# Optimization experiments

Hardware: AMD Instinct MI355X
Metric: run time of the kernel (lower is better)

Reference implementation:

```python
import jax, jax.numpy as jnp
import numpy as np

N, E, DIN, DH, DOUT, NB = 50000, 400000, 32, 128, 16, 2

def setup_inputs() -> dict:
    key = jax.random.key(0)
    ks = jax.random.split(key, 16)
    s = 0.05
    inp = {
        "inputs": jax.random.normal(ks[0], (N, DIN), jnp.float32),
        "frames": jax.random.normal(ks[1], (N, 3, 3), jnp.float32),
        "edge_index": jax.random.randint(ks[2], (2, E), 0, N, jnp.int32),
        # GraphNet in/out projections
        "win": jax.random.normal(ks[3], (DIN, DH), jnp.float32) * s,
        "bin_": jnp.zeros((DH,), jnp.float32),
        "wout": jax.random.normal(ks[4], (DH, DOUT), jnp.float32) * s,
        "bout": jnp.zeros((DOUT,), jnp.float32),
        # per-block EdgeConv params, stacked over NB blocks
        # mlp1: Linear(2*DH, DH) -> ReLU -> Linear(DH, DH) -> ReLU -> Linear(DH, DH)
        "w1a": jax.random.normal(ks[5], (NB, 2 * DH, DH), jnp.float32) * s,
        "b1a": jnp.zeros((NB, DH), jnp.float32),
        "w1b": jax.random.normal(ks[6], (NB, DH, DH), jnp.float32) * s,
        "b1b": jnp.zeros((NB, DH), jnp.float32),
        "w1c": jax.random.normal(ks[7], (NB, DH, DH), jnp.float32) * s,
        "b1c": jnp.zeros((NB, DH), jnp.float32),
        # mlp2: Linear(DH, DH) -> ReLU -> Linear(DH, DH)
        "w2a": jax.random.normal(ks[8], (NB, DH, DH), jnp.float32) * s,
        "b2a": jnp.zeros((NB, DH), jnp.float32),
        "w2b": jax.random.normal(ks[9], (NB, DH, DH), jnp.float32) * s,
        "b2b": jnp.zeros((NB, DH), jnp.float32),
    }
    return inp


def reference(inputs, frames, edge_index, win, bin_, wout, bout,
              w1a, b1a, w1b, b1b, w1c, b1c, w2a, b2a, w2b, b2b):
    src = edge_index[0]  # j: message source
    dst = edge_index[1]  # i: aggregation target (PyG convention)
    x = inputs @ win + bin_  # [N, DH]
    for b in range(NB):
        x_j = x[src]  # [E, DH] gather
        x_i = x[dst]  # [E, DH] gather
        m = jnp.concatenate([x_j, x_i], axis=-1)  # [E, 2*DH]
        m = jax.nn.relu(m @ w1a[b] + b1a[b])
        m = jax.nn.relu(m @ w1b[b] + b1b[b])
        m = m @ w1c[b] + b1c[b]  # [E, DH]
        agg = jax.ops.segment_sum(m, dst, num_segments=N)  # aggr='add'
        h = jax.nn.relu(agg @ w2a[b] + b2a[b])
        x = h @ w2b[b] + b2b[b]
    return x @ wout + bout  # [N, DOUT]
```

## Files before the change

kernel.cpp:

```cpp
#include <hip/hip_runtime.h>

#define NN 50000
#define NE 400000
#define DIN 32
#define DH  128
#define DOUT 16
#define NB  2
#define NBLK 49
#define NTILE (NE / 64)

typedef _Float16 half8 __attribute__((ext_vector_type(8)));
typedef _Float16 half4 __attribute__((ext_vector_type(4)));
typedef float    f32x4 __attribute__((ext_vector_type(4)));

#define FENCE() asm volatile("s_waitcnt lgkmcnt(0)" ::: "memory")
#define MFMA16(a, b, c) __builtin_amdgcn_mfma_f32_16x16x32_f16((a), (b), (c), 0, 0, 0)

__global__ void k_node_proj(const float* __restrict__ inp,
                            const float* __restrict__ win,
                            const float* __restrict__ bin,
                            _Float16* __restrict__ x16) {
    int gid = blockIdx.x * blockDim.x + threadIdx.x;
    if (gid >= NN * DH) return;
    int n = gid >> 7, h = gid & 127;
    float acc = bin[h];
    const float* row = inp + (size_t)n * DIN;
#pragma unroll
    for (int k = 0; k < DIN; ++k) acc = fmaf(row[k], win[k * DH + h], acc);
    x16[gid] = (_Float16)acc;
}

__global__ void k_wprep(const float* __restrict__ w1a, const float* __restrict__ w1b,
                        const float* __restrict__ w1c, const float* __restrict__ w2a,
                        const float* __restrict__ w2b, _Float16* __restrict__ wf) {
    int c = blockIdx.x * blockDim.x + threadIdx.x;
    if (c >= NB * 12288) return;
    int b = c / 12288, r = c % 12288;
    int tt = r >> 9, rem = r & 511;
    const float* W; int t;
    if (tt < 8)       { W = w1a + (size_t)b * 2 * DH * DH; t = tt; }
    else if (tt < 12) { W = w1b + (size_t)b * DH * DH; t = tt - 8; }
    else if (tt < 16) { W = w1c + (size_t)b * DH * DH; t = tt - 12; }
    else if (tt < 20) { W = w2a + (size_t)b * DH * DH; t = tt - 16; }
    else              { W = w2b + (size_t)b * DH * DH; t = tt - 20; }
    bool perm = (tt >= 12 && tt < 16);
    int n = rem >> 6, l = rem & 63;
    int col = n * 16 + (l & 15);
    half8 v;
#pragma unroll
    for (int j = 0; j < 8; ++j) {
        int row = perm ? ((2 * t + (j >> 2)) * 16 + (l >> 4) * 4 + (j & 3))
                       : (t * 32 + (l >> 4) * 8 + j);
        v[j] = (_Float16)W[(size_t)row * DH + col];
    }
    *(half8*)(wf + (size_t)c * 8) = v;
}

__global__ void k_woutprep(const float* __restrict__ wout, _Float16* __restrict__ wf) {
    int c = threadIdx.x;
    int t = c >> 6, l = c & 63;
    half8 v;
#pragma unroll
    for (int j = 0; j < 8; ++j)
        v[j] = (_Float16)wout[(size_t)(t * 32 + (l >> 4) * 8 + j) * DOUT + (l & 15)];
    *(half8*)(wf + (size_t)c * 8) = v;
}

__global__ void k_hist(const int* __restrict__ dstI, int* __restrict__ deg) {
    int e = blockIdx.x * blockDim.x + threadIdx.x;
    if (e < NE) atomicAdd(&deg[dstI[e]], 1);
}

__global__ void __launch_bounds__(1024) k_scanA(const int* __restrict__ deg,
                                                int* __restrict__ bsum) {
    __shared__ int ws[16];
    int tid = threadIdx.x, wv = tid >> 6, l = tid & 63;
    int i = blockIdx.x * 1024 + tid;
    int v = (i < NN) ? deg[i] : 0;
#pragma unroll
    for (int off = 32; off; off >>= 1) v += __shfl_down(v, off);
    if (l == 0) ws[wv] = v;
    __syncthreads();
    if (tid == 0) {
        int s = 0;
#pragma unroll
        for (int k = 0; k < 16; ++k) s += ws[k];
        bsum[blockIdx.x] = s;
    }
}

__global__ void k_scanB(const int* __restrict__ bsum, int* __restrict__ boff) {
    int l = threadIdx.x;
    int v = (l < NBLK) ? bsum[l] : 0;
    int s = v;
#pragma unroll
    for (int off = 1; off < 64; off <<= 1) {
        int t = __shfl_up(s, off);
        if (l >= off) s += t;
    }
    if (l < NBLK) boff[l] = s - v;
}

__global__ void __launch_bounds__(1024) k_scanC(const int* __restrict__ deg,
                                                const int* __restrict__ boff,
                                                int* __restrict__ cur) {
    __shared__ int ws[16];
    int tid = threadIdx.x, wv = tid >> 6, l = tid & 63;
    int i = blockIdx.x * 1024 + tid;
    int v = (i < NN) ? deg[i] : 0;
    int s = v;
#pragma unroll
    for (int off = 1; off < 64; off <<= 1) {
        int t = __shfl_up(s, off);
        if (l >= off) s += t;
    }
    if (l == 63) ws[wv] = s;
    __syncthreads();
    if (wv == 0) {
        int t = (l < 16) ? ws[l] : 0;
#pragma unroll
        for (int off = 1; off < 16; off <<= 1) {
            int u = __shfl_up(t, off);
            if (l >= off) t += u;
        }
        if (l < 16) ws[l] = t;
    }
    __syncthreads();
    int base = boff[blockIdx.x] + (wv ? ws[wv - 1] : 0);
    if (i < NN) cur[i] = base + s - v;
}

__global__ void k_scatter(const int* __restrict__ srcI, const int* __restrict__ dstI,
                          int* __restrict__ cur, int* __restrict__ eS,
                          int* __restrict__ eD) {
    int e = blockIdx.x * blockDim.x + threadIdx.x;
    if (e >= NE) return;
    int d = dstI[e];
    int p = atomicAdd(&cur[d], 1);
    eS[p] = srcI[e];
    eD[p] = d;
}

__global__ void __launch_bounds__(256, 4) k_y(
    const _Float16* __restrict__ x,
    const half8* __restrict__ wfa, const float* __restrict__ b1a,
    _Float16* __restrict__ yj, _Float16* __restrict__ yi) {
    const int tid = threadIdx.x, wv = tid >> 6, l = tid & 63;
    const int lm = l & 15, lk = l >> 4;
    const int n0 = (blockIdx.x * 4 + wv) * 16;
    if (n0 >= NN) return;
    int node = n0 + lm;
    if (node >= NN) node = NN - 1;

    const f32x4 z = {0.f, 0.f, 0.f, 0.f};
    f32x4 aj[8], ai[8];
#pragma unroll
    for (int n = 0; n < 8; ++n) { aj[n] = z; ai[n] = z; }
#pragma unroll
    for (int t = 0; t < 4; ++t) {
        half8 a = *(const half8*)(x + (size_t)node * DH + t * 32 + lk * 8);
#pragma unroll
        for (int n = 0; n < 8; ++n) {
            aj[n] = MFMA16(a, wfa[(size_t)(t * 8 + n) * 64 + l], aj[n]);
            ai[n] = MFMA16(a, wfa[(size_t)((t + 4) * 8 + n) * 64 + l], ai[n]);
        }
    }
#pragma unroll
    for (int n = 0; n < 8; ++n) {
        float bi = b1a[n * 16 + lm];
#pragma unroll
        for (int r = 0; r < 4; ++r) {
            int nd = n0 + lk * 4 + r;
            if (nd < NN) {
                yj[(size_t)nd * DH + n * 16 + lm] = (_Float16)aj[n][r];
                yi[(size_t)nd * DH + n * 16 + lm] = (_Float16)(ai[n][r] + bi);
            }
        }
    }
}

__global__ void __launch_bounds__(256, 3) k_edge10(
    const _Float16* __restrict__ yj, const _Float16* __restrict__ yi,
    const int* __restrict__ eS, const int* __restrict__ eD,
    const half8* __restrict__ wfb, const half8* __restrict__ wfc,
    const float* __restrict__ b1b,
    float* __restrict__ agg) {
    __shared__ _Float16 smAll[4][4096];
    __shared__ int slotT[4][16];

    const int tid = threadIdx.x, wv = tid >> 6, l = tid & 63;
    const int lm = l & 15, lk = l >> 4;

    int bid = blockIdx.x;
    int xcd = bid & 7, idx = bid >> 3;
    int tile = (xcd < 2 ? xcd * 782 : 2 * 782 + (xcd - 2) * 781) + idx;
    const int ebase = tile * 64 + wv * 16;

    const int src = eS[ebase + lm];
    const int dst = eD[ebase + lm];

    _Float16* sm = smAll[wv];
    if (lk >= 2) {
        half8 zz;
#pragma unroll
        for (int j = 0; j < 8; ++j) zz[j] = (_Float16)0.f;
#pragma unroll
        for (int g = 0; g < 8; ++g) *(half8*)&sm[(g * 64 + l) * 8] = zz;
    }

    int dprev = __shfl(dst, (l & 48) | ((lm - 1) & 15));
    bool bit = (lm == 0) || (dst != dprev);
    unsigned mask16 = (unsigned)__ballot(bit) & 0xFFFFu;
    int slot_l = __popc(mask16 & ((2u << lm) - 1)) - 1;
    int nsl = __popc(mask16);
    if (l < 16 && bit) slotT[wv][slot_l] = dst;

    half4 bb[8];
#pragma unroll
    for (int n = 0; n < 8; ++n) {
        float4 bf = *(const float4*)(b1b + n * 16 + lk * 4);
#pragma unroll
        for (int r = 0; r < 4; ++r) bb[n][r] = (_Float16)(&bf.x)[r];
    }

    const f32x4 z = {0.f, 0.f, 0.f, 0.f};
    f32x4 acc[8];
#pragma unroll
    for (int n = 0; n < 8; ++n) acc[n] = z;

#pragma unroll
    for (int t = 0; t < 4; ++t) {
        half8 ya = *(const half8*)(yj + (size_t)src * DH + t * 32 + lk * 8);
        half8 yb = *(const half8*)(yi + (size_t)dst * DH + t * 32 + lk * 8);
        half8 m1;
#pragma unroll
        for (int j = 0; j < 8; ++j) {
            _Float16 v = ya[j] + yb[j];
            m1[j] = v > (_Float16)0.f ? v : (_Float16)0.f;
        }
#pragma unroll
        for (int n = 0; n < 8; ++n)
            acc[n] = MFMA16(wfb[(size_t)(t * 8 + n) * 64 + l], m1, acc[n]);
    }

    f32x4 ac3[8];
#pragma unroll
    for (int n = 0; n < 8; ++n) ac3[n] = z;
#pragma unroll
    for (int t = 0; t < 4; ++t) {
        half8 b3;
#pragma unroll
        for (int j = 0; j < 8; ++j) {
            int n2 = 2 * t + (j >> 2), r = j & 3;
            float v = acc[n2][r] + (float)bb[n2][r];
            b3[j] = (_Float16)fmaxf(v, 0.f);
        }
#pragma unroll
        for (int n = 0; n < 8; ++n)
            ac3[n] = MFMA16(wfc[(size_t)(t * 8 + n) * 64 + l], b3, ac3[n]);
    }

#pragma unroll
    for (int n = 0; n < 8; ++n)
#pragma unroll
        for (int r = 0; r < 4; ++r)
            sm[(n * 64 + (lm >> 3) * 16 + lk * 4 + r) * 8 + (lm & 7)] =
                (_Float16)ac3[n][r];
    FENCE();

    half8 ind;
#pragma unroll
    for (int e8 = 0; e8 < 8; ++e8) {
        int ks = lk * 8 + e8;
        int se = __shfl(slot_l, ks & 15);
        ind[e8] = (ks < 16 && se == lm) ? (_Float16)1.f : (_Float16)0.f;
    }
    int4 dv = *(const int4*)&slotT[wv][lk * 4];
#pragma unroll
    for (int g = 0; g < 8; ++g) {
        half8 bf = *(const half8*)&sm[(g * 64 + l) * 8];
        f32x4 p = MFMA16(ind, bf, z);
#pragma unroll
        for (int r = 0; r < 4; ++r) {
            int s0 = lk * 4 + r;
            if (s0 < nsl)
                unsafeAtomicAdd(agg + (size_t)(&dv.x)[r] * DH + g * 16 + lm, p[r]);
        }
    }
}

template <int MODE>
__global__ void __launch_bounds__(256, 3) k_node10(
    const float* __restrict__ agg, const int* __restrict__ deg,
    const float* __restrict__ b1c,
    const half8* __restrict__ w2af, const half8* __restrict__ w2bf,
    const float* __restrict__ b2a, const float* __restrict__ b2b,
    const half8* __restrict__ wfaN, const float* __restrict__ b1aN,
    _Float16* __restrict__ yj, _Float16* __restrict__ yi,
    const half8* __restrict__ woutf, const float* __restrict__ bout,
    float* __restrict__ out) {
    __shared__ _Float16 sM[4][2048];
    const int tid = threadIdx.x, wv = tid >> 6, l = tid & 63;
    const int lm = l & 15, lk = l >> 4;
    const int n0 = (blockIdx.x * 4 + wv) * 16;
    if (n0 >= NN) return;
    int nodeA = n0 + lm;
    if (nodeA >= NN) nodeA = NN - 1;
    const float degf = (float)deg[nodeA];

    float b2ar[8], b2br[8];
#pragma unroll
    for (int n = 0; n < 8; ++n) {
        b2ar[n] = b2a[n * 16 + lm];
        b2br[n] = b2b[n * 16 + lm];
    }

    const f32x4 z = {0.f, 0.f, 0.f, 0.f};
    f32x4 acc[8];
#pragma unroll
    for (int n = 0; n < 8; ++n) acc[n] = z;

    for (int t = 0; t < 4; ++t) {
        const float* ap = agg + (size_t)nodeA * DH + t * 32 + lk * 8;
        float4 v0 = *(const float4*)ap;
        float4 v1 = *(const float4*)(ap + 4);
        float4 c0 = *(const float4*)(b1c + t * 32 + lk * 8);
        float4 c1 = *(const float4*)(b1c + t * 32 + lk * 8 + 4);
        half8 a;
#pragma unroll
        for (int j = 0; j < 4; ++j) {
            a[j]     = (_Float16)((&v0.x)[j] + degf * (&c0.x)[j]);
            a[4 + j] = (_Float16)((&v1.x)[j] + degf * (&c1.x)[j]);
        }
        const half8* wp = w2af + (size_t)t * 512 + l;
#pragma unroll
        for (int n = 0; n < 8; ++n) acc[n] = MFMA16(a, wp[n * 64], acc[n]);
    }
    _Float16* sm = sM[wv];
#pragma unroll
    for (int n = 0; n < 8; ++n) {
        int base = ((n >> 1) * 64 + ((n & 1) * 2 + (lm >> 3)) * 16 + lk * 4) * 8 +
                   (lm & 7);
#pragma unroll
        for (int j = 0; j < 4; ++j)
            sm[base + j * 8] = (_Float16)fmaxf(acc[n][j] + b2ar[n], 0.f);
    }
    FENCE();
#pragma unroll
    for (int n = 0; n < 8; ++n) acc[n] = z;
    for (int t = 0; t < 4; ++t) {
        half8 a = *(const half8*)&sm[(t * 64 + l) * 8];
        const half8* wp = w2bf + (size_t)t * 512 + l;
#pragma unroll
        for (int n = 0; n < 8; ++n) acc[n] = MFMA16(a, wp[n * 64], acc[n]);
    }
    FENCE();
#pragma unroll
    for (int n = 0; n < 8; ++n) {
        int base = ((n >> 1) * 64 + ((n & 1) * 2 + (lm >> 3)) * 16 + lk * 4) * 8 +
                   (lm & 7);
#pragma unroll
        for (int j = 0; j < 4; ++j)
            sm[base + j * 8] = (_Float16)(acc[n][j] + b2br[n]);
    }
    FENCE();

    if (MODE == 0) {
        f32x4 aj[8], ai[8];
#pragma unroll
        for (int n = 0; n < 8; ++n) { aj[n] = z; ai[n] = z; }
#pragma unroll
        for (int t = 0; t < 4; ++t) {
            half8 a = *(const half8*)&sm[(t * 64 + l) * 8];
#pragma unroll
            for (int n = 0; n < 8; ++n) {
                aj[n] = MFMA16(a, wfaN[(size_t)(t * 8 + n) * 64 + l], aj[n]);
                ai[n] = MFMA16(a, wfaN[(size_t)((t + 4) * 8 + n) * 64 + l], ai[n]);
            }
        }
#pragma unroll
        for (int n = 0; n < 8; ++n) {
            float bi = b1aN[n * 16 + lm];
#pragma unroll
            for (int r = 0; r < 4; ++r) {
                int nd = n0 + lk * 4 + r;
                if (nd < NN) {
                    yj[(size_t)nd * DH + n * 16 + lm] = (_Float16)aj[n][r];
                    yi[(size_t)nd * DH + n * 16 + lm] = (_Float16)(ai[n][r] + bi);
                }
            }
        }
    } else {
        f32x4 ao = z;
        for (int t = 0; t < 4; ++t) {
            half8 a = *(const half8*)&sm[(t * 64 + l) * 8];
            ao = MFMA16(a, woutf[t * 64 + l], ao);
        }
        float bo = bout[lm];
#pragma unroll
        for (int j = 0; j < 4; ++j) {
            int nd = n0 + lk * 4 + j;
            if (nd < NN) out[(size_t)nd * DOUT + lm] = ao[j] + bo;
        }
    }
}

extern "C" void kernel_launch(void* const* d_in, const int* in_sizes, int n_in,
                              void* d_out, int out_size, void* d_ws, size_t ws_size,
                              hipStream_t stream) {
    const float* inputs = (const float*)d_in[0];
    const int* eidx = (const int*)d_in[2];
    const int* srcI = eidx;
    const int* dstI = eidx + NE;
    const float* win  = (const float*)d_in[3];
    const float* bin_ = (const float*)d_in[4];
    const float* wout = (const float*)d_in[5];
    const float* bout = (const float*)d_in[6];
    const float* w1a = (const float*)d_in[7];
    const float* b1a = (const float*)d_in[8];
    const float* w1b = (const float*)d_in[9];
    const float* b1b = (const float*)d_in[10];
    const float* w1c = (const float*)d_in[11];
    const float* b1c = (const float*)d_in[12];
    const float* w2a = (const float*)d_in[13];
    const float* b2a = (const float*)d_in[14];
    const float* w2b = (const float*)d_in[15];
    const float* b2b = (const float*)d_in[16];

    char* p = (char*)d_ws;
    _Float16* xa = (_Float16*)p;    p += (size_t)NN * DH * 2;
    _Float16* yj = (_Float16*)p;    p += (size_t)NN * DH * 2;
    _Float16* yi = (_Float16*)p;    p += (size_t)NN * DH * 2;
    _Float16* wfAll = (_Float16*)p; p += ((size_t)NB * 12288 + 256) * 16;
    float* agg   = (float*)p;       p += (size_t)NN * DH * 4;
    int* deg     = (int*)p;         p += (size_t)NN * 4;
    int* cur     = (int*)p;         p += (size_t)NN * 4;
    int* bsum    = (int*)p;         p += 256;
    int* boff    = (int*)p;         p += 256;
    int* eSrt    = (int*)p;         p += (size_t)NE * 4;
    int* eDrt    = (int*)p;         p += (size_t)NE * 4;
    float* out   = (float*)d_out;
    _Float16* wfW = wfAll + (size_t)NB * 12288 * 8;

    const half8* wb0 = (const half8*)wfAll;
    const half8* wb1 = (const half8*)(wfAll + (size_t)12288 * 8);

    k_wprep<<<(NB * 12288 + 255) / 256, 256, 0, stream>>>(w1a, w1b, w1c, w2a, w2b, wfAll);
    k_woutprep<<<1, 256, 0, stream>>>(wout, wfW);
    k_node_proj<<<(NN * DH + 255) / 256, 256, 0, stream>>>(inputs, win, bin_, xa);

    hipMemsetAsync(deg, 0, (size_t)NN * 4, stream);
    k_hist<<<(NE + 255) / 256, 256, 0, stream>>>(dstI, deg);
    k_scanA<<<NBLK, 1024, 0, stream>>>(deg, bsum);
    k_scanB<<<1, 64, 0, stream>>>(bsum, boff);
    k_scanC<<<NBLK, 1024, 0, stream>>>(deg, boff, cur);
    k_scatter<<<(NE + 255) / 256, 256, 0, stream>>>(srcI, dstI, cur, eSrt, eDrt);

    const int NWGN = (NN + 63) / 64;
    k_y<<<NWGN, 256, 0, stream>>>(xa, wb0, b1a, yj, yi);
    hipMemsetAsync(agg, 0, (size_t)NN * DH * 4, stream);
    k_edge10<<<NTILE, 256, 0, stream>>>(yj, yi, eSrt, eDrt,
                                        wb0 + 4096, wb0 + 6144, b1b, agg);
    k_node10<0><<<NWGN, 256, 0, stream>>>(
        agg, deg, b1c, wb0 + 8192, wb0 + 10240, b2a, b2b,
        wb1, b1a + DH, yj, yi, nullptr, nullptr, nullptr);
    hipMemsetAsync(agg, 0, (size_t)NN * DH * 4, stream);
    k_edge10<<<NTILE, 256, 0, stream>>>(yj, yi, eSrt, eDrt,
                                        wb1 + 4096, wb1 + 6144, b1b + DH, agg);
    k_node10<1><<<NWGN, 256, 0, stream>>>(
        agg, deg, b1c + DH, wb1 + 8192, wb1 + 10240, b2a + DH, b2b + DH,
        nullptr, nullptr, nullptr, nullptr, (const half8*)wfW, bout, out);
}
```

Measured before the change: 359.7 us.

## Fuse prep kernels, fold input projection into k_y, zero agg in node pass

Merges the weight prep, wout prep, a new win-to-fp16 fragment prep and the degree histogram into a single k_prep launch. The fp32 input projection kernel and its xa buffer are removed. The projection is now done with MFMA inside k_y0 and staged through shared memory, so the fp16 x array no longer goes through global memory. k_node10<0> zeroes agg as it reads it, which drops the second memset, and k_edge10's launch bounds rise to 4 waves per SIMD, which may cause register spills.

```diff
diff --git a/kernel.cpp b/kernel.cpp
--- a/kernel.cpp
+++ b/kernel.cpp
@@ -16,59 +16,53 @@
 #define FENCE() asm volatile("s_waitcnt lgkmcnt(0)" ::: "memory")
 #define MFMA16(a, b, c) __builtin_amdgcn_mfma_f32_16x16x32_f16((a), (b), (c), 0, 0, 0)
 
-__global__ void k_node_proj(const float* __restrict__ inp,
-                            const float* __restrict__ win,
-                            const float* __restrict__ bin,
-                            _Float16* __restrict__ x16) {
-    int gid = blockIdx.x * blockDim.x + threadIdx.x;
-    if (gid >= NN * DH) return;
-    int n = gid >> 7, h = gid & 127;
-    float acc = bin[h];
-    const float* row = inp + (size_t)n * DIN;
-#pragma unroll
-    for (int k = 0; k < DIN; ++k) acc = fmaf(row[k], win[k * DH + h], acc);
-    x16[gid] = (_Float16)acc;
-}
-
-__global__ void k_wprep(const float* __restrict__ w1a, const float* __restrict__ w1b,
-                        const float* __restrict__ w1c, const float* __restrict__ w2a,
-                        const float* __restrict__ w2b, _Float16* __restrict__ wf) {
-    int c = blockIdx.x * blockDim.x + threadIdx.x;
-    if (c >= NB * 12288) return;
-    int b = c / 12288, r = c % 12288;
-    int tt = r >> 9, rem = r & 511;
-    const float* W; int t;
-    if (tt < 8)       { W = w1a + (size_t)b * 2 * DH * DH; t = tt; }
-    else if (tt < 12) { W = w1b + (size_t)b * DH * DH; t = tt - 8; }
-    else if (tt < 16) { W = w1c + (size_t)b * DH * DH; t = tt - 12; }
-    else if (tt < 20) { W = w2a + (size_t)b * DH * DH; t = tt - 16; }
-    else              { W = w2b + (size_t)b * DH * DH; t = tt - 20; }
-    bool perm = (tt >= 12 && tt < 16);
-    int n = rem >> 6, l = rem & 63;
-    int col = n * 16 + (l & 15);
-    half8 v;
-#pragma unroll
-    for (int j = 0; j < 8; ++j) {
-        int row = perm ? ((2 * t + (j >> 2)) * 16 + (l >> 4) * 4 + (j & 3))
-                       : (t * 32 + (l >> 4) * 8 + j);
-        v[j] = (_Float16)W[(size_t)row * DH + col];
-    }
-    *(half8*)(wf + (size_t)c * 8) = v;
-}
-
-__global__ void k_woutprep(const float* __restrict__ wout, _Float16* __restrict__ wf) {
-    int c = threadIdx.x;
-    int t = c >> 6, l = c & 63;
-    half8 v;
-#pragma unroll
-    for (int j = 0; j < 8; ++j)
-        v[j] = (_Float16)wout[(size_t)(t * 32 + (l >> 4) * 8 + j) * DOUT + (l & 15)];
-    *(half8*)(wf + (size_t)c * 8) = v;
-}
-
-__global__ void k_hist(const int* __restrict__ dstI, int* __restrict__ deg) {
-    int e = blockIdx.x * blockDim.x + threadIdx.x;
-    if (e < NE) atomicAdd(&deg[dstI[e]], 1);
+__global__ void k_prep(const float* __restrict__ w1a, const float* __restrict__ w1b,
+                       const float* __restrict__ w1c, const float* __restrict__ w2a,
+                       const float* __restrict__ w2b, const float* __restrict__ wout,
+                       const float* __restrict__ win, const int* __restrict__ dstI,
+                       _Float16* __restrict__ wf, int* __restrict__ deg) {
+    const int b = blockIdx.x, tid = threadIdx.x;
+    if (b < (NB * 12288) / 256) {
+        int c = b * 256 + tid;
+        int bb = c / 12288, r = c % 12288;
+        int tt = r >> 9, rem = r & 511;
+        const float* W; int t;
+        if (tt < 8)       { W = w1a + (size_t)bb * 2 * DH * DH; t = tt; }
+        else if (tt < 12) { W = w1b + (size_t)bb * DH * DH; t = tt - 8; }
+        else if (tt < 16) { W = w1c + (size_t)bb * DH * DH; t = tt - 12; }
+        else if (tt < 20) { W = w2a + (size_t)bb * DH * DH; t = tt - 16; }
+        else              { W = w2b + (size_t)bb * DH * DH; t = tt - 20; }
+        bool perm = (tt >= 12 && tt < 16);
+        int n = rem >> 6, l = rem & 63;
+        int col = n * 16 + (l & 15);
+        half8 v;
+#pragma unroll
+        for (int j = 0; j < 8; ++j) {
+            int row = perm ? ((2 * t + (j >> 2)) * 16 + (l >> 4) * 4 + (j & 3))
+                           : (t * 32 + (l >> 4) * 8 + j);
+            v[j] = (_Float16)W[(size_t)row * DH + col];
+        }
+        *(half8*)(wf + (size_t)c * 8) = v;
+    } else if (b == 96) {
+        int c = tid;
+        int t = c >> 6, l = c & 63;
+        half8 v;
+#pragma unroll
+        for (int j = 0; j < 8; ++j)
+            v[j] = (_Float16)wout[(size_t)(t * 32 + (l >> 4) * 8 + j) * DOUT + (l & 15)];
+        *(half8*)(wf + (size_t)(NB * 12288 + c) * 8) = v;
+    } else if (b < 99) {
+        int c = (b - 97) * 256 + tid;
+        int n = c >> 6, l = c & 63;
+        half8 v;
+#pragma unroll
+        for (int j = 0; j < 8; ++j)
+            v[j] = (_Float16)win[(size_t)((l >> 4) * 8 + j) * DH + n * 16 + (l & 15)];
+        *(half8*)(wf + (size_t)(NB * 12288 + 256 + c) * 8) = v;
+    } else {
+        int e = (b - 99) * 256 + tid;
+        if (e < NE) atomicAdd(&deg[dstI[e]], 1);
+    }
 }
 
 __global__ void __launch_bounds__(1024) k_scanA(const int* __restrict__ deg,
@@ -141,10 +135,12 @@
     eD[p] = d;
 }
 
-__global__ void __launch_bounds__(256, 4) k_y(
-    const _Float16* __restrict__ x,
+__global__ void __launch_bounds__(256, 4) k_y0(
+    const float* __restrict__ inp,
+    const half8* __restrict__ winf, const float* __restrict__ bin,
     const half8* __restrict__ wfa, const float* __restrict__ b1a,
     _Float16* __restrict__ yj, _Float16* __restrict__ yi) {
+    __shared__ _Float16 sM[4][2048];
     const int tid = threadIdx.x, wv = tid >> 6, l = tid & 63;
     const int lm = l & 15, lk = l >> 4;
     const int n0 = (blockIdx.x * 4 + wv) * 16;
@@ -153,12 +149,41 @@
     if (node >= NN) node = NN - 1;
 
     const f32x4 z = {0.f, 0.f, 0.f, 0.f};
+    half8 a0;
+    {
+        const float* ip = inp + (size_t)node * DIN + lk * 8;
+        float4 v0 = *(const float4*)ip;
+        float4 v1 = *(const float4*)(ip + 4);
+#pragma unroll
+        for (int j = 0; j < 4; ++j) {
+            a0[j]     = (_Float16)(&v0.x)[j];
+            a0[4 + j] = (_Float16)(&v1.x)[j];
+        }
+    }
+    f32x4 xacc[8];
+#pragma unroll
+    for (int n = 0; n < 8; ++n) xacc[n] = z;
+#pragma unroll
+    for (int n = 0; n < 8; ++n) xacc[n] = MFMA16(a0, winf[n * 64 + l], xacc[n]);
+
+    _Float16* sm = sM[wv];
+#pragma unroll
+    for (int n = 0; n < 8; ++n) {
+        float bi = bin[n * 16 + lm];
+        int base = ((n >> 1) * 64 + ((n & 1) * 2 + (lm >> 3)) * 16 + lk * 4) * 8 +
+                   (lm & 7);
+#pragma unroll
+        for (int j = 0; j < 4; ++j)
+            sm[base + j * 8] = (_Float16)(xacc[n][j] + bi);
+    }
+    FENCE();
+
     f32x4 aj[8], ai[8];
 #pragma unroll
     for (int n = 0; n < 8; ++n) { aj[n] = z; ai[n] = z; }
 #pragma unroll
     for (int t = 0; t < 4; ++t) {
-        half8 a = *(const half8*)(x + (size_t)node * DH + t * 32 + lk * 8);
+        half8 a = *(const half8*)&sm[(t * 64 + l) * 8];
 #pragma unroll
         for (int n = 0; n < 8; ++n) {
             aj[n] = MFMA16(a, wfa[(size_t)(t * 8 + n) * 64 + l], aj[n]);
@@ -179,7 +204,7 @@
     }
 }
 
-__global__ void __launch_bounds__(256, 3) k_edge10(
+__global__ void __launch_bounds__(256, 4) k_edge10(
     const _Float16* __restrict__ yj, const _Float16* __restrict__ yi,
     const int* __restrict__ eS, const int* __restrict__ eD,
     const half8* __restrict__ wfb, const half8* __restrict__ wfc,
@@ -291,7 +316,7 @@
 
 template <int MODE>
 __global__ void __launch_bounds__(256, 3) k_node10(
-    const float* __restrict__ agg, const int* __restrict__ deg,
+    float* __restrict__ agg, const int* __restrict__ deg,
     const float* __restrict__ b1c,
     const half8* __restrict__ w2af, const half8* __restrict__ w2bf,
     const float* __restrict__ b2a, const float* __restrict__ b2b,
@@ -321,9 +346,14 @@
     for (int n = 0; n < 8; ++n) acc[n] = z;
 
     for (int t = 0; t < 4; ++t) {
-        const float* ap = agg + (size_t)nodeA * DH + t * 32 + lk * 8;
+        float* ap = agg + (size_t)nodeA * DH + t * 32 + lk * 8;
         float4 v0 = *(const float4*)ap;
         float4 v1 = *(const float4*)(ap + 4);
+        if (MODE == 0) {
+            float4 z4 = make_float4(0.f, 0.f, 0.f, 0.f);
+            *(float4*)ap = z4;
+            *(float4*)(ap + 4) = z4;
+        }
         float4 c0 = *(const float4*)(b1c + t * 32 + lk * 8);
         float4 c1 = *(const float4*)(b1c + t * 32 + lk * 8 + 4);
         half8 a;
@@ -428,10 +458,9 @@
     const float* b2b = (const float*)d_in[16];
 
     char* p = (char*)d_ws;
-    _Float16* xa = (_Float16*)p;    p += (size_t)NN * DH * 2;
     _Float16* yj = (_Float16*)p;    p += (size_t)NN * DH * 2;
     _Float16* yi = (_Float16*)p;    p += (size_t)NN * DH * 2;
-    _Float16* wfAll = (_Float16*)p; p += ((size_t)NB * 12288 + 256) * 16;
+    _Float16* wfAll = (_Float16*)p; p += ((size_t)NB * 12288 + 768) * 16;
     float* agg   = (float*)p;       p += (size_t)NN * DH * 4;
     int* deg     = (int*)p;         p += (size_t)NN * 4;
     int* cur     = (int*)p;         p += (size_t)NN * 4;
@@ -440,34 +469,31 @@
     int* eSrt    = (int*)p;         p += (size_t)NE * 4;
     int* eDrt    = (int*)p;         p += (size_t)NE * 4;
     float* out   = (float*)d_out;
-    _Float16* wfW = wfAll + (size_t)NB * 12288 * 8;
 
     const half8* wb0 = (const half8*)wfAll;
     const half8* wb1 = (const half8*)(wfAll + (size_t)12288 * 8);
-
-    k_wprep<<<(NB * 12288 + 255) / 256, 256, 0, stream>>>(w1a, w1b, w1c, w2a, w2b, wfAll);
-    k_woutprep<<<1, 256, 0, stream>>>(wout, wfW);
-    k_node_proj<<<(NN * DH + 255) / 256, 256, 0, stream>>>(inputs, win, bin_, xa);
+    const half8* wfW = (const half8*)(wfAll + (size_t)NB * 12288 * 8);
+    const half8* wfI = (const half8*)(wfAll + (size_t)(NB * 12288 + 256) * 8);
 
     hipMemsetAsync(deg, 0, (size_t)NN * 4, stream);
-    k_hist<<<(NE + 255) / 256, 256, 0, stream>>>(dstI, deg);
+    k_prep<<<99 + (NE + 255) / 256, 256, 0, stream>>>(
+        w1a, w1b, w1c, w2a, w2b, wout, win, dstI, wfAll, deg);
     k_scanA<<<NBLK, 1024, 0, stream>>>(deg, bsum);
     k_scanB<<<1, 64, 0, stream>>>(bsum, boff);
     k_scanC<<<NBLK, 1024, 0, stream>>>(deg, boff, cur);
     k_scatter<<<(NE + 255) / 256, 256, 0, stream>>>(srcI, dstI, cur, eSrt, eDrt);
 
     const int NWGN = (NN + 63) / 64;
-    k_y<<<NWGN, 256, 0, stream>>>(xa, wb0, b1a, yj, yi);
+    k_y0<<<NWGN, 256, 0, stream>>>(inputs, wfI, bin_, wb0, b1a, yj, yi);
     hipMemsetAsync(agg, 0, (size_t)NN * DH * 4, stream);
     k_edge10<<<NTILE, 256, 0, stream>>>(yj, yi, eSrt, eDrt,
                                         wb0 + 4096, wb0 + 6144, b1b, agg);
     k_node10<0><<<NWGN, 256, 0, stream>>>(
         agg, deg, b1c, wb0 + 8192, wb0 + 10240, b2a, b2b,
         wb1, b1a + DH, yj, yi, nullptr, nullptr, nullptr);
-    hipMemsetAsync(agg, 0, (size_t)NN * DH * 4, stream);
     k_edge10<<<NTILE, 256, 0, stream>>>(yj, yi, eSrt, eDrt,
                                         wb1 + 4096, wb1 + 6144, b1b + DH, agg);
     k_node10<1><<<NWGN, 256, 0, stream>>>(
         agg, deg, b1c + DH, wb1 + 8192, wb1 + 10240, b2a + DH, b2b + DH,
-        nullptr, nullptr, nullptr, nullptr, (const half8*)wfW, bout, out);
-}
+        nullptr, nullptr, nullptr, nullptr, wfW, bout, out);
+}
```

Result: no change. 359.8 us (+0.0%).
